# Performance work log

Hardware: AMD Instinct MI355X
Metric: run time of the kernel (lower is better)

Reference implementation:

```python
import jax, jax.numpy as jnp
import numpy as np

EPS = 1e-5

def bitlinear158(x, W):
    # BitNet b1.58 weight ternarization: beta = 1/mean(|W|), w_q = round(W*beta).clamp(-1,1)/beta
    beta = 1.0 / jnp.clip(jnp.mean(jnp.abs(W)), EPS, None)
    w_q = jnp.clip(jnp.round(W * beta), -1.0, 1.0) / beta
    # straight-through estimator (no-op in pure forward, kept for faithfulness)
    w = W + jax.lax.stop_gradient(w_q - W)
    return x @ w.T

def lrelu(x):
    return jnp.where(x >= 0, x, 0.2 * x)

def setup_inputs() -> dict:
    key = jax.random.key(0)
    ks = jax.random.split(key, 12)
    B, D_IN, H, L, Z = 65536, 784, 400, 200, 2
    def w(k, fan_out, fan_in):
        bound = 1.0 / np.sqrt(fan_in)
        return jax.random.uniform(k, (fan_out, fan_in), jnp.float32, -bound, bound)
    return {
        "x": jax.random.uniform(ks[0], (B, D_IN), jnp.float32),
        "epsilon": jax.random.normal(ks[1], (B, Z), jnp.float32),
        "W_e1": w(ks[2], H, D_IN),
        "W_e2": w(ks[3], H, H),
        "W_e3": w(ks[4], L, H),
        "W_mu": w(ks[5], Z, L),
        "W_lv": w(ks[6], Z, L),
        "W_d1": w(ks[7], L, Z),
        "W_d2": w(ks[8], H, L),
        "W_d3": w(ks[9], H, H),
        "W_d4": w(ks[10], H, H),
        "W_d5": w(ks[11], D_IN, H),
    }

def reference(x, epsilon, W_e1, W_e2, W_e3, W_mu, W_lv, W_d1, W_d2, W_d3, W_d4, W_d5):
    # encoder
    h = lrelu(bitlinear158(x, W_e1))
    h = lrelu(bitlinear158(h, W_e2))
    h = lrelu(bitlinear158(h, W_e3))
    mean = bitlinear158(h, W_mu)
    logvar = bitlinear158(h, W_lv)
    # reparameterization (source uses logvar directly as 'var')
    z = mean + logvar * epsilon
    # decoder
    d = lrelu(bitlinear158(z, W_d1))
    d = lrelu(bitlinear158(d, W_d2))
    d = lrelu(bitlinear158(d, W_d3))
    d = lrelu(bitlinear158(d, W_d4))
    x_hat = jax.nn.sigmoid(bitlinear158(d, W_d5))
    return (x_hat, mean, logvar)
```

## Files before the change

### kernel.cpp

```cpp
#include <hip/hip_runtime.h>

using u16 = unsigned short;
using u32 = unsigned int;

typedef __attribute__((ext_vector_type(8))) short bf16x8;
typedef __attribute__((ext_vector_type(4))) float f32x4;
typedef __attribute__((ext_vector_type(8))) u16 u16x8;

static __device__ __forceinline__ float b2f(u16 u) {
  return __uint_as_float((u32)u << 16);
}
static __device__ __forceinline__ u16 f2b(float f) {
  u32 x = __float_as_uint(f);
  return (u16)((x + 0x7fffu + ((x >> 16) & 1u)) >> 16);
}
static __device__ __forceinline__ void gload_lds16(const void* g, void* l) {
  __builtin_amdgcn_global_load_lds(
      (const __attribute__((address_space(1))) void*)g,
      (__attribute__((address_space(3))) void*)l, 16, 0, 0);
}

struct WMeta {
  const float* src;
  u16* dst;
  int N, K, Np, Kp, scaleIdx, blockStart;
};
struct PrepArgs { WMeta w[10]; };

__global__ __launch_bounds__(256)
void absmean_part(PrepArgs pa, double* __restrict__ partials)
{
  const int w = blockIdx.x >> 6;
  const int p = blockIdx.x & 63;
  const WMeta mw = pa.w[w];
  const long n = (long)mw.N * mw.K;
  const long chunk = (n + 63) >> 6;
  const long lo = (long)p * chunk;
  const long hi = min(n, lo + chunk);
  double sum = 0.0;
  for (long i = lo + threadIdx.x; i < hi; i += 256)
    sum += (double)fabsf(mw.src[i]);
  __shared__ double red[256];
  red[threadIdx.x] = sum;
  __syncthreads();
  for (int off = 128; off > 0; off >>= 1) {
    if (threadIdx.x < off) red[threadIdx.x] += red[threadIdx.x + off];
    __syncthreads();
  }
  if (threadIdx.x == 0) partials[blockIdx.x] = red[0];
}

__global__ __launch_bounds__(64)
void absmean_final(PrepArgs pa, const double* __restrict__ partials,
                   float* __restrict__ scales)
{
  const int w = threadIdx.x;
  if (w < 10) {
    double s = 0.0;
    #pragma unroll
    for (int i = 0; i < 64; ++i) s += partials[(w << 6) + i];
    const WMeta mw = pa.w[w];
    double m = s / (double)((long)mw.N * mw.K);
    scales[mw.scaleIdx] = (float)fmax(m, 1e-5);
  }
}

__global__ __launch_bounds__(256)
void ternarize_k(PrepArgs pa, const float* __restrict__ scales)
{
  const int b = blockIdx.x;
  int w = 0;
  #pragma unroll
  for (int i = 1; i < 10; ++i) if (b >= pa.w[i].blockStart) w = i;
  const WMeta mw = pa.w[w];
  const float inv = 1.0f / scales[mw.scaleIdx];
  const int tot = mw.Np * mw.Kp;
  int idx = (b - mw.blockStart) * 2048 + threadIdx.x * 8;
  #pragma unroll
  for (int j = 0; j < 8; ++j, ++idx) {
    if (idx < tot) {
      const int nn = idx / mw.Kp;
      const int kk = idx - nn * mw.Kp;
      float v = 0.f;
      if (nn < mw.N && kk < mw.K) {
        float t = rintf(mw.src[(size_t)nn * mw.K + kk] * inv);
        v = fminf(1.f, fmaxf(-1.f, t));
      }
      mw.dst[idx] = f2b(v);
    }
  }
}

__global__ __launch_bounds__(256)
void convert_x(const float* __restrict__ x, u16* __restrict__ xb)
{
  const int s = blockIdx.x * 256 + threadIdx.x;
  const int row = s / 112;
  const int c8 = s - row * 112;
  u16x8 o = (u16x8)(u16)0;
  if (c8 < 98) {
    const float4* px = (const float4*)(x + (size_t)row * 784 + c8 * 8);
    float4 v0 = px[0], v1 = px[1];
    o[0] = f2b(v0.x); o[1] = f2b(v0.y); o[2] = f2b(v0.z); o[3] = f2b(v0.w);
    o[4] = f2b(v1.x); o[5] = f2b(v1.y); o[6] = f2b(v1.z); o[7] = f2b(v1.w);
  }
  *(u16x8*)(xb + (size_t)row * 896 + c8 * 8) = o;
}

template<bool LRELU, bool SIGMOID, bool OUTBF16>
__global__ __launch_bounds__(512, 6)
void gemm_t(const u16* __restrict__ A, const u16* __restrict__ Bw,
            void* __restrict__ Out, const float* __restrict__ sptr,
            int Kp, int ldOut, int Nstore)
{
  __shared__ __align__(16) u16 lds[3 * 8192];
  const int tid = threadIdx.x;
  const int lane = tid & 63, wid = tid >> 6;
  const int wr = wid >> 2, wc = wid & 3;

  const u32 bid = blockIdx.y * gridDim.x + blockIdx.x;
  const u32 cpx = (gridDim.x * gridDim.y) >> 3;
  const u32 wg = (bid & 7) * cpx + (bid >> 3);
  const int m0 = (int)(wg / gridDim.x) << 7;
  const int n0 = (int)(wg % gridDim.x) << 7;
  const int NT = Kp >> 5;

  const int srow = tid >> 2;
  const int sk = (((tid & 3) ^ ((tid >> 3) & 3)) << 3);
  const size_t gA0 = (size_t)(m0 + srow) * Kp + sk;
  const size_t gB0 = (size_t)(n0 + srow) * Kp + sk;
  const int ldst = wid << 9;

  auto stage = [&](int kt, int slot) {
    u16* base = lds + slot * 8192;
    const int ke = kt << 5;
    gload_lds16(A + gA0 + ke, base + ldst);
    gload_lds16(Bw + gB0 + ke, base + 4096 + ldst);
  };

  const int cs = (((lane >> 4) ^ ((lane >> 1) & 3)) << 4);
  int offA[4], offB[2];
  #pragma unroll
  for (int m = 0; m < 4; ++m)
    offA[m] = ((wr << 6) + (m << 4) + (lane & 15)) * 64 + cs;
  #pragma unroll
  for (int n = 0; n < 2; ++n)
    offB[n] = ((wc << 5) + (n << 4) + (lane & 15)) * 64 + cs + 8192;

  f32x4 acc[4][2] = {};
  stage(0, 0);
  stage(1, 1);
  int slot = 0;
  for (int kt = 0; kt < NT; ++kt) {
    asm volatile("s_waitcnt lgkmcnt(0)" ::: "memory");
    __builtin_amdgcn_s_barrier();
    asm volatile("" ::: "memory");
    int st2 = slot + 2; if (st2 >= 3) st2 -= 3;
    if (kt + 2 < NT) {
      stage(kt + 2, st2);
      asm volatile("s_waitcnt vmcnt(4)" ::: "memory");
    } else if (kt + 1 < NT) {
      asm volatile("s_waitcnt vmcnt(2)" ::: "memory");
    } else {
      asm volatile("s_waitcnt vmcnt(0)" ::: "memory");
    }
    __builtin_amdgcn_s_barrier();
    asm volatile("" ::: "memory");

    const char* lbase = (const char*)(lds + slot * 8192);
    bf16x8 av[4], bv[2];
    #pragma unroll
    for (int m = 0; m < 4; ++m) av[m] = *(const bf16x8*)(lbase + offA[m]);
    #pragma unroll
    for (int n = 0; n < 2; ++n) bv[n] = *(const bf16x8*)(lbase + offB[n]);
    __builtin_amdgcn_s_setprio(1);
    #pragma unroll
    for (int m = 0; m < 4; ++m)
      #pragma unroll
      for (int n = 0; n < 2; ++n)
        acc[m][n] = __builtin_amdgcn_mfma_f32_16x16x32_bf16(av[m], bv[n], acc[m][n], 0, 0, 0);
    __builtin_amdgcn_s_setprio(0);
    slot = (slot == 2) ? 0 : slot + 1;
  }

  const float s = *sptr;
  #pragma unroll
  for (int n = 0; n < 2; ++n) {
    const int col = n0 + (wc << 5) + (n << 4) + (lane & 15);
    if (col >= Nstore) continue;
    #pragma unroll
    for (int m = 0; m < 4; ++m) {
      const int row0 = m0 + (wr << 6) + (m << 4) + ((lane >> 4) << 2);
      #pragma unroll
      for (int r = 0; r < 4; ++r) {
        float v = acc[m][n][r] * s;
        if (LRELU)   v = v >= 0.f ? v : 0.2f * v;
        if (SIGMOID) v = 1.f / (1.f + __expf(-v));
        if (OUTBF16) ((u16*)Out)[(size_t)(row0 + r) * ldOut + col] = f2b(v);
        else         ((float*)Out)[(size_t)(row0 + r) * ldOut + col] = v;
      }
    }
  }
}

__global__ __launch_bounds__(256)
void mid_kernel(const u16* __restrict__ h3, const u16* __restrict__ wmulv,
                const u16* __restrict__ wd1, const float* __restrict__ eps,
                float* __restrict__ outMean, float* __restrict__ outLv,
                u16* __restrict__ hd1, const float* __restrict__ scales)
{
  __shared__ __align__(16) u16 wML[1024];
  __shared__ u32 wD1s[256];
  __shared__ float zz[64][2];
  const int tid = threadIdx.x;
  if (tid < 128) ((u16x8*)wML)[tid] = ((const u16x8*)wmulv)[tid];
  wD1s[tid] = ((const u32*)wd1)[tid];
  __syncthreads();
  const float smu = scales[3], slv = scales[4], sd1 = scales[5];
  const int rl = tid >> 2, q = tid & 3;
  const size_t row = (size_t)blockIdx.x * 64 + rl;
  float a0 = 0.f, a1 = 0.f, a2 = 0.f, a3 = 0.f;
  const u16* hrow = h3 + row * 256 + q * 64;
  #pragma unroll
  for (int k8 = 0; k8 < 8; ++k8) {
    u16x8 hv = *(const u16x8*)(hrow + k8 * 8);
    u16x8 w0 = *(const u16x8*)(wML +   0 + q * 64 + k8 * 8);
    u16x8 w1 = *(const u16x8*)(wML + 256 + q * 64 + k8 * 8);
    u16x8 w2 = *(const u16x8*)(wML + 512 + q * 64 + k8 * 8);
    u16x8 w3 = *(const u16x8*)(wML + 768 + q * 64 + k8 * 8);
    #pragma unroll
    for (int j = 0; j < 8; ++j) {
      const float hf = b2f(hv[j]);
      a0 += hf * b2f(w0[j]);
      a1 += hf * b2f(w1[j]);
      a2 += hf * b2f(w2[j]);
      a3 += hf * b2f(w3[j]);
    }
  }
  a0 += __shfl_xor(a0, 1); a0 += __shfl_xor(a0, 2);
  a1 += __shfl_xor(a1, 1); a1 += __shfl_xor(a1, 2);
  a2 += __shfl_xor(a2, 1); a2 += __shfl_xor(a2, 2);
  a3 += __shfl_xor(a3, 1); a3 += __shfl_xor(a3, 2);
  if (q == 0) {
    const float m0v = a0 * smu, m1v = a1 * smu;
    const float l0v = a2 * slv, l1v = a3 * slv;
    const float e0 = eps[row * 2], e1 = eps[row * 2 + 1];
    outMean[row * 2]     = m0v; outMean[row * 2 + 1] = m1v;
    outLv[row * 2]       = l0v; outLv[row * 2 + 1]   = l1v;
    zz[rl][0] = m0v + l0v * e0;
    zz[rl][1] = m1v + l1v * e1;
  }
  __syncthreads();
  const u32 wp = wD1s[tid];
  const float t0 = b2f((u16)(wp & 0xffffu));
  const float t1 = b2f((u16)(wp >> 16));
  const bool live = tid < 200;
  u16* ocol = hd1 + ((size_t)blockIdx.x * 64) * 256 + tid;
  #pragma unroll 4
  for (int it = 0; it < 64; ++it) {
    float v = live ? sd1 * (zz[it][0] * t0 + zz[it][1] * t1) : 0.f;
    v = v >= 0.f ? v : 0.2f * v;
    ocol[(size_t)it * 256] = f2b(v);
  }
}

extern "C" void kernel_launch(void* const* d_in, const int* in_sizes, int n_in,
                              void* d_out, int out_size, void* d_ws, size_t ws_size,
                              hipStream_t stream)
{
  (void)in_sizes; (void)n_in; (void)out_size; (void)ws_size;
  const float* x   = (const float*)d_in[0];
  const float* eps = (const float*)d_in[1];
  float* out_f = (float*)d_out;

  float* scales = (float*)d_ws;
  u16* wb = (u16*)((char*)d_ws + 256);
  constexpr size_t E1 = 0;
  constexpr size_t E2 = 458752;
  constexpr size_t E3 = 720896;
  constexpr size_t MULV = 851968;
  constexpr size_t D1 = 852992;
  constexpr size_t D2 = 853504;
  constexpr size_t D3 = 984576;
  constexpr size_t D4 = 1246720;
  constexpr size_t D5 = 1508864;
  constexpr size_t WTOT = 2033152;
  u16* bufA = (u16*)((char*)d_ws + 256 + WTOT * 2);
  u16* bufB = (u16*)((char*)bufA + (size_t)65536 * 896 * 2);
  double* partials = (double*)bufA;

  PrepArgs pa;
  auto setw = [&](int i, int di, size_t off, int N, int K, int Np, int Kp, int bs) {
    pa.w[i] = WMeta{ (const float*)d_in[di], wb + off, N, K, Np, Kp, i, bs };
  };
  setw(0,  2, E1,        400, 784, 512, 896,   0);
  setw(1,  3, E2,        400, 400, 512, 512, 224);
  setw(2,  4, E3,        200, 400, 256, 512, 352);
  setw(3,  5, MULV,        2, 200,   2, 256, 416);
  setw(4,  6, MULV + 512,  2, 200,   2, 256, 417);
  setw(5,  7, D1,        200,   2, 256,   2, 418);
  setw(6,  8, D2,        400, 200, 512, 256, 419);
  setw(7,  9, D3,        400, 400, 512, 512, 483);
  setw(8, 10, D4,        400, 400, 512, 512, 611);
  setw(9, 11, D5,        784, 400,1024, 512, 739);

  absmean_part<<<640, 256, 0, stream>>>(pa, partials);
  absmean_final<<<1, 64, 0, stream>>>(pa, partials, scales);
  ternarize_k<<<995, 256, 0, stream>>>(pa, scales);
  convert_x<<<28672, 256, 0, stream>>>(x, bufA);

  dim3 blk(512);
  gemm_t<true , false, true ><<<dim3(4, 512), blk, 0, stream>>>(bufA, wb + E1, bufB, scales + 0, 896, 512, 512);
  gemm_t<true , false, true ><<<dim3(4, 512), blk, 0, stream>>>(bufB, wb + E2, bufA, scales + 1, 512, 512, 512);
  gemm_t<true , false, true ><<<dim3(2, 512), blk, 0, stream>>>(bufA, wb + E3, bufB, scales + 2, 512, 256, 256);
  mid_kernel<<<1024, 256, 0, stream>>>(bufB, wb + MULV, wb + D1, eps,
                                       out_f + (size_t)65536 * 784,
                                       out_f + (size_t)65536 * 784 + 131072,
                                       bufA, scales);
  gemm_t<true , false, true ><<<dim3(4, 512), blk, 0, stream>>>(bufA, wb + D2, bufB, scales + 6, 256, 512, 512);
  gemm_t<true , false, true ><<<dim3(4, 512), blk, 0, stream>>>(bufB, wb + D3, bufA, scales + 7, 512, 512, 512);
  gemm_t<true , false, true ><<<dim3(4, 512), blk, 0, stream>>>(bufA, wb + D4, bufB, scales + 8, 512, 512, 512);
  gemm_t<false, true , false><<<dim3(8, 512), blk, 0, stream>>>(bufB, wb + D5, (void*)out_f, scales + 9, 512, 784, 784);
}
```

Before: 770.1 us.

## Enlarge GEMM tiles to 256x256 with K=64 and quadrant-phased double buffering

Replaces the 128x128x32 triple-buffered GEMM with a 256x256 tile over a 64-wide K step. Each K step runs four quadrant phases, and each phase prefetches one quarter of the next stage into a double-buffered LDS region. The aim is to raise arithmetic intensity and cut global/LDS traffic per MFMA while spreading loads across the phases. In exchange, each block holds 128 accumulator registers and 128KB of LDS, which lowers occupancy to roughly one block per CU and reduces the number of blocks for small GEMMs like E3.

```diff
diff --git a/kernel.cpp b/kernel.cpp
--- a/kernel.cpp
+++ b/kernel.cpp
@@ -108,12 +108,12 @@
 }
 
 template<bool LRELU, bool SIGMOID, bool OUTBF16>
-__global__ __launch_bounds__(512, 6)
-void gemm_t(const u16* __restrict__ A, const u16* __restrict__ Bw,
+__global__ __launch_bounds__(512, 2)
+void gemm8p(const u16* __restrict__ A, const u16* __restrict__ Bw,
             void* __restrict__ Out, const float* __restrict__ sptr,
             int Kp, int ldOut, int Nstore)
 {
-  __shared__ __align__(16) u16 lds[3 * 8192];
+  __shared__ __align__(16) u16 lds[2 * 4 * 8192];
   const int tid = threadIdx.x;
   const int lane = tid & 63, wid = tid >> 6;
   const int wr = wid >> 2, wc = wid & 3;
@@ -121,79 +121,104 @@
   const u32 bid = blockIdx.y * gridDim.x + blockIdx.x;
   const u32 cpx = (gridDim.x * gridDim.y) >> 3;
   const u32 wg = (bid & 7) * cpx + (bid >> 3);
-  const int m0 = (int)(wg / gridDim.x) << 7;
-  const int n0 = (int)(wg % gridDim.x) << 7;
-  const int NT = Kp >> 5;
-
-  const int srow = tid >> 2;
-  const int sk = (((tid & 3) ^ ((tid >> 3) & 3)) << 3);
-  const size_t gA0 = (size_t)(m0 + srow) * Kp + sk;
-  const size_t gB0 = (size_t)(n0 + srow) * Kp + sk;
+  const int m0 = (int)(wg / gridDim.x) << 8;
+  const int n0 = (int)(wg % gridDim.x) << 8;
+  const int NT = Kp >> 6;
+
+  const int srow = tid >> 3;
+  const int sk = (((tid & 7) ^ (srow & 7)) << 3);
   const int ldst = wid << 9;
-
-  auto stage = [&](int kt, int slot) {
-    u16* base = lds + slot * 8192;
-    const int ke = kt << 5;
-    gload_lds16(A + gA0 + ke, base + ldst);
-    gload_lds16(Bw + gB0 + ke, base + 4096 + ldst);
+  auto stage_half = [&](int tau, int b, int s) {
+    const u16* src = (s < 2) ? A : Bw;
+    const int rbase = ((s < 2) ? m0 : n0) + ((s & 1) << 7) + srow;
+    const size_t kb = ((size_t)tau << 6) + sk;
+    u16* d = lds + (b << 15) + (s << 13) + ldst;
+    gload_lds16(src + (size_t)rbase * Kp + kb, d);
+    gload_lds16(src + (size_t)(rbase + 64) * Kp + kb, d + 4096);
   };
 
-  const int cs = (((lane >> 4) ^ ((lane >> 1) & 3)) << 4);
-  int offA[4], offB[2];
-  #pragma unroll
-  for (int m = 0; m < 4; ++m)
-    offA[m] = ((wr << 6) + (m << 4) + (lane & 15)) * 64 + cs;
-  #pragma unroll
-  for (int n = 0; n < 2; ++n)
-    offB[n] = ((wc << 5) + (n << 4) + (lane & 15)) * 64 + cs + 8192;
-
-  f32x4 acc[4][2] = {};
-  stage(0, 0);
-  stage(1, 1);
-  int slot = 0;
-  for (int kt = 0; kt < NT; ++kt) {
-    asm volatile("s_waitcnt lgkmcnt(0)" ::: "memory");
-    __builtin_amdgcn_s_barrier();
-    asm volatile("" ::: "memory");
-    int st2 = slot + 2; if (st2 >= 3) st2 -= 3;
-    if (kt + 2 < NT) {
-      stage(kt + 2, st2);
-      asm volatile("s_waitcnt vmcnt(4)" ::: "memory");
-    } else if (kt + 1 < NT) {
-      asm volatile("s_waitcnt vmcnt(2)" ::: "memory");
-    } else {
-      asm volatile("s_waitcnt vmcnt(0)" ::: "memory");
+  const int rlaneA = (wr << 6) + (lane & 15);
+  const int rlaneB = (wc << 5) + (lane & 15);
+  const int swz0 = (((lane >> 4)) ^ (lane & 7)) << 4;
+  const int swz1 = ((4 + (lane >> 4)) ^ (lane & 7)) << 4;
+  const int baseA0 = rlaneA * 128 + swz0, baseA1 = rlaneA * 128 + swz1;
+  const int baseB0 = rlaneB * 128 + swz0, baseB1 = rlaneB * 128 + swz1;
+
+  f32x4 acc[8][4] = {};
+
+  stage_half(0, 0, 0);
+  stage_half(0, 0, 2);
+  stage_half(0, 0, 3);
+  stage_half(0, 0, 1);
+
+  for (int t = 0; t < NT; ++t) {
+    const int pb = t & 1;
+    const bool pref = (t + 1 < NT);
+    const int sb = pb ^ 1;
+
+#define GPHASE(QM, QN, SSLOT, WMAIN, WLAST)                                     \
+    {                                                                           \
+      if (pref) {                                                               \
+        stage_half(t + 1, sb, SSLOT);                                           \
+        if ((WMAIN) >= 0)                                                       \
+          asm volatile("s_waitcnt vmcnt(%0)" :: "i"(WMAIN) : "memory");         \
+      } else {                                                                  \
+        if ((WLAST) >= 0)                                                       \
+          asm volatile("s_waitcnt vmcnt(%0)" :: "i"(WLAST) : "memory");         \
+      }                                                                         \
+      __builtin_amdgcn_s_barrier();                                             \
+      asm volatile("" ::: "memory");                                            \
+      const char* pA = (const char*)(lds + (pb << 15) + ((QM) << 13));          \
+      const char* pB = (const char*)(lds + (pb << 15) + ((2 + (QN)) << 13));    \
+      bf16x8 av[4][2], bv[2][2];                                                \
+      _Pragma("unroll")                                                         \
+      for (int mf = 0; mf < 4; ++mf) {                                          \
+        av[mf][0] = *(const bf16x8*)(pA + baseA0 + (mf << 11));                 \
+        av[mf][1] = *(const bf16x8*)(pA + baseA1 + (mf << 11));                 \
+      }                                                                         \
+      _Pragma("unroll")                                                         \
+      for (int nf = 0; nf < 2; ++nf) {                                          \
+        bv[nf][0] = *(const bf16x8*)(pB + baseB0 + (nf << 11));                 \
+        bv[nf][1] = *(const bf16x8*)(pB + baseB1 + (nf << 11));                 \
+      }                                                                         \
+      __builtin_amdgcn_s_setprio(1);                                            \
+      _Pragma("unroll")                                                         \
+      for (int mf = 0; mf < 4; ++mf)                                            \
+        _Pragma("unroll")                                                       \
+        for (int nf = 0; nf < 2; ++nf) {                                        \
+          acc[((QM)<<2)+mf][((QN)<<1)+nf] =                                     \
+            __builtin_amdgcn_mfma_f32_16x16x32_bf16(av[mf][0], bv[nf][0],       \
+                acc[((QM)<<2)+mf][((QN)<<1)+nf], 0, 0, 0);                      \
+          acc[((QM)<<2)+mf][((QN)<<1)+nf] =                                     \
+            __builtin_amdgcn_mfma_f32_16x16x32_bf16(av[mf][1], bv[nf][1],       \
+                acc[((QM)<<2)+mf][((QN)<<1)+nf], 0, 0, 0);                      \
+        }                                                                       \
+      __builtin_amdgcn_s_setprio(0);                                            \
     }
-    __builtin_amdgcn_s_barrier();
-    asm volatile("" ::: "memory");
-
-    const char* lbase = (const char*)(lds + slot * 8192);
-    bf16x8 av[4], bv[2];
-    #pragma unroll
-    for (int m = 0; m < 4; ++m) av[m] = *(const bf16x8*)(lbase + offA[m]);
-    #pragma unroll
-    for (int n = 0; n < 2; ++n) bv[n] = *(const bf16x8*)(lbase + offB[n]);
-    __builtin_amdgcn_s_setprio(1);
-    #pragma unroll
-    for (int m = 0; m < 4; ++m)
-      #pragma unroll
-      for (int n = 0; n < 2; ++n)
-        acc[m][n] = __builtin_amdgcn_mfma_f32_16x16x32_bf16(av[m], bv[n], acc[m][n], 0, 0, 0);
-    __builtin_amdgcn_s_setprio(0);
-    slot = (slot == 2) ? 0 : slot + 1;
+
+    GPHASE(0, 0, 0, 6, 4)
+    GPHASE(0, 1, 2, 6, 2)
+    GPHASE(1, 0, 3, 6, 0)
+    GPHASE(1, 1, 1, -1, -1)
+#undef GPHASE
   }
 
   const float s = *sptr;
   #pragma unroll
-  for (int n = 0; n < 2; ++n) {
-    const int col = n0 + (wc << 5) + (n << 4) + (lane & 15);
+  for (int qn = 0; qn < 2; ++qn)
+  #pragma unroll
+  for (int nf = 0; nf < 2; ++nf) {
+    const int col = n0 + (qn << 7) + (wc << 5) + (nf << 4) + (lane & 15);
     if (col >= Nstore) continue;
     #pragma unroll
-    for (int m = 0; m < 4; ++m) {
-      const int row0 = m0 + (wr << 6) + (m << 4) + ((lane >> 4) << 2);
+    for (int qm = 0; qm < 2; ++qm)
+    #pragma unroll
+    for (int mf = 0; mf < 4; ++mf) {
+      const int row0 = m0 + (qm << 7) + (wr << 6) + (mf << 4) + ((lane >> 4) << 2);
+      const f32x4 a = acc[(qm << 2) + mf][(qn << 1) + nf];
       #pragma unroll
       for (int r = 0; r < 4; ++r) {
-        float v = acc[m][n][r] * s;
+        float v = a[r] * s;
         if (LRELU)   v = v >= 0.f ? v : 0.2f * v;
         if (SIGMOID) v = 1.f / (1.f + __expf(-v));
         if (OUTBF16) ((u16*)Out)[(size_t)(row0 + r) * ldOut + col] = f2b(v);
@@ -310,15 +335,15 @@
   convert_x<<<28672, 256, 0, stream>>>(x, bufA);
 
   dim3 blk(512);
-  gemm_t<true , false, true ><<<dim3(4, 512), blk, 0, stream>>>(bufA, wb + E1, bufB, scales + 0, 896, 512, 512);
-  gemm_t<true , false, true ><<<dim3(4, 512), blk, 0, stream>>>(bufB, wb + E2, bufA, scales + 1, 512, 512, 512);
-  gemm_t<true , false, true ><<<dim3(2, 512), blk, 0, stream>>>(bufA, wb + E3, bufB, scales + 2, 512, 256, 256);
+  gemm8p<true , false, true ><<<dim3(2, 256), blk, 0, stream>>>(bufA, wb + E1, bufB, scales + 0, 896, 512, 512);
+  gemm8p<true , false, true ><<<dim3(2, 256), blk, 0, stream>>>(bufB, wb + E2, bufA, scales + 1, 512, 512, 512);
+  gemm8p<true , false, true ><<<dim3(1, 256), blk, 0, stream>>>(bufA, wb + E3, bufB, scales + 2, 512, 256, 256);
   mid_kernel<<<1024, 256, 0, stream>>>(bufB, wb + MULV, wb + D1, eps,
                                        out_f + (size_t)65536 * 784,
                                        out_f + (size_t)65536 * 784 + 131072,
                                        bufA, scales);
-  gemm_t<true , false, true ><<<dim3(4, 512), blk, 0, stream>>>(bufA, wb + D2, bufB, scales + 6, 256, 512, 512);
-  gemm_t<true , false, true ><<<dim3(4, 512), blk, 0, stream>>>(bufB, wb + D3, bufA, scales + 7, 512, 512, 512);
-  gemm_t<true , false, true ><<<dim3(4, 512), blk, 0, stream>>>(bufA, wb + D4, bufB, scales + 8, 512, 512, 512);
-  gemm_t<false, true , false><<<dim3(8, 512), blk, 0, stream>>>(bufB, wb + D5, (void*)out_f, scales + 9, 512, 784, 784);
-}
+  gemm8p<true , false, true ><<<dim3(2, 256), blk, 0, stream>>>(bufA, wb + D2, bufB, scales + 6, 256, 512, 512);
+  gemm8p<true , false, true ><<<dim3(2, 256), blk, 0, stream>>>(bufB, wb + D3, bufA, scales + 7, 512, 512, 512);
+  gemm8p<true , false, true ><<<dim3(2, 256), blk, 0, stream>>>(bufA, wb + D4, bufB, scales + 8, 512, 512, 512);
+  gemm8p<false, true , false><<<dim3(4, 256), blk, 0, stream>>>(bufB, wb + D5, (void*)out_f, scales + 9, 512, 784, 784);
+}
```

New measurement: 753.3 us. 2.2% less time.
